# Optimization experiments

Hardware: AMD Instinct MI355X
Metric: run time of the kernel (lower is better)

## Reference

```python
import jax, jax.numpy as jnp
import numpy as np

DEPTH = 16
PERCENT = 1.2
MAX_P = 5.0
# ps[t] = clip((t+1)*percent, 0, max_percent), as in the torch __init__
PS = np.clip((np.arange(DEPTH) + 1) * PERCENT, 0.0, MAX_P)


def setup_inputs() -> dict:
    key = jax.random.key(0)
    kx, kA = jax.random.split(key, 2)
    B, M, N = 16384, 256, 1024
    A = jax.random.normal(kA, (M, N), dtype=jnp.float32) / np.sqrt(M)
    # L = max eigenvalue of A^T A (as max_eig in the torch code), scaled by 1.001
    gram = np.asarray(A.T @ A)
    L = float(np.linalg.eigvalsh(gram)[-1]) * 1.001
    # init=True initialization: every bias layer weight is A.T / L, threshold = 1/L
    W = jnp.tile((A.T / L)[None, :, :], (DEPTH, 1, 1))  # [depth, N, M]
    threshold = jnp.ones((DEPTH,), dtype=jnp.float32) / L
    x = jax.random.normal(kx, (B, M), dtype=jnp.float32)
    return {"x": x, "A": A, "W": W, "threshold": threshold}


def _shrink(x, t):
    # soft threshold: sign(x) * max(|x| - t, 0)
    return jnp.sign(x) * jnp.maximum(jnp.abs(x) - t, 0.0)


def _shrinkss(x, t, p):
    # support-selection shrink: entries above both the learned threshold and the
    # per-row (100-p) percentile of |x| pass through untouched; the rest are
    # soft-thresholded. Mask and percentile are detached (no_grad in torch).
    n = x.shape[1]
    idx = int(np.ceil((100.0 - p) / 100.0 * n)) - 1  # static per iteration
    abs_x = jnp.abs(x)
    thresh = jax.lax.stop_gradient(jnp.sort(abs_x, axis=1)[:, idx])  # [B]
    mask = jax.lax.stop_gradient(
        ((abs_x >= t) & (abs_x >= thresh[:, None])).astype(x.dtype)
    )
    return mask * x + _shrink((1.0 - mask) * x, t)


def reference(x, A, W, threshold):
    # x: [B, M], A: [M, N], W: [depth, N, M], threshold: [depth]
    B = x.shape[0]
    N = A.shape[1]
    u = jnp.zeros((B, N), dtype=x.dtype)
    for i in range(DEPTH):
        r = x - u @ A.T                      # residual in measurement space [B, M]
        v = u + r @ W[i].T                   # gradient step via learned bias [B, N]
        u = _shrinkss(v, threshold[i], PS[i])
    return u
```

## Files before the change

kernel.cpp:

```cpp
#include <hip/hip_runtime.h>
#include <hip/hip_bf16.h>

#define B_ROWS 16384
#define M_DIM  256
#define N_DIM  1024
#define DEPTH  16

typedef __attribute__((ext_vector_type(8))) short short8;
typedef __attribute__((ext_vector_type(4))) float f32x4;
typedef __attribute__((ext_vector_type(2))) float f32x2;

#define ATP_OFF_B   0
#define WTP_OFF_B   1572864
#define RP_OFF_B    (1572864 + 25165824)
#define TAU_OFF_B   (RP_OFF_B + 25165824)
#define WS_FAST_NEED ((size_t)TAU_OFF_B + 65536)
#define WTP_SLICE   (64 * 8 * 3 * 512)
#define RP_PANEL_US 24576

#define AT_OFF 0
#define WT_OFF (262144)
#define WS_OLD_NEED ((size_t)(262144 + 16 * 262144) * 4)

__device__ __forceinline__ unsigned short bf16r(float f) {
    unsigned u = __float_as_uint(f);
    u += 0x7fffu + ((u >> 16) & 1u);
    return (unsigned short)(u >> 16);
}
__device__ __forceinline__ float bf2f(unsigned short h) {
    return __uint_as_float(((unsigned)h) << 16);
}
__device__ __forceinline__ void split3(float x, unsigned short& h, unsigned short& m,
                                       unsigned short& lo) {
    h = bf16r(x); float r1 = x - bf2f(h);
    m = bf16r(r1); float r2 = r1 - bf2f(m);
    lo = bf16r(r2);
}
__device__ __forceinline__ f32x4 MF(short8 a, short8 b, f32x4 c) {
    return __builtin_amdgcn_mfma_f32_16x16x32_bf16(a, b, c, 0, 0, 0);
}
__device__ __forceinline__ float shrink_one(float v, float t, float thrv) {
    float a = fabsf(v);
    return (a >= thrv) ? v : copysignf(fmaxf(a - t, 0.0f), v);
}

__global__ void prep_a_kernel(const float* __restrict__ A, unsigned short* __restrict__ ATp) {
    int g = blockIdx.x * 256 + threadIdx.x;
    if (g >= 16 * 32 * 64) return;
    int l = g & 63, kc = (g >> 6) & 31, tile = g >> 11;
    int row = tile * 16 + (l & 15);
    int k0 = kc * 32 + ((l >> 4) << 3);
    unsigned short h[8], m[8], lo[8];
#pragma unroll
    for (int j = 0; j < 8; ++j) split3(A[(size_t)row * N_DIM + k0 + j], h[j], m[j], lo[j]);
    size_t base = ((size_t)(tile * 32 + kc) * 3) * 512 + l * 8;
#pragma unroll
    for (int j = 0; j < 8; ++j) {
        ATp[base + j] = h[j];
        ATp[base + 512 + j] = m[j];
        ATp[base + 1024 + j] = lo[j];
    }
}

__global__ void prep_w_kernel(const float* __restrict__ W, unsigned short* __restrict__ WTp) {
    int g = blockIdx.x * 256 + threadIdx.x;
    if (g >= 16 * 64 * 8 * 64) return;
    int l = g & 63, kc = (g >> 6) & 7, tile = (g >> 9) & 63, it = g >> 15;
    int n = tile * 16 + (l & 15);
    int m0 = kc * 32 + ((l >> 4) << 3);
    const float* Wi = W + (size_t)it * N_DIM * M_DIM;
    unsigned short h[8], m[8], lo[8];
#pragma unroll
    for (int j = 0; j < 8; ++j) split3(Wi[(size_t)n * M_DIM + m0 + j], h[j], m[j], lo[j]);
    size_t base = (((size_t)(it * 64 + tile) * 8 + kc) * 3) * 512 + l * 8;
#pragma unroll
    for (int j = 0; j < 8; ++j) {
        WTp[base + j] = h[j];
        WTp[base + 512 + j] = m[j];
        WTp[base + 1024 + j] = lo[j];
    }
}

__global__ void prep_x_kernel(const float* __restrict__ x, unsigned short* __restrict__ RP) {
    int g = blockIdx.x * 256 + threadIdx.x;
    if (g >= 524288) return;
    int l = g & 63, kcp = (g >> 6) & 3, wm = (g >> 8) & 1, c = (g >> 9) & 1, panel = g >> 10;
    int row = panel * 32 + wm * 16 + (l & 15);
    int k0 = c * 128 + kcp * 32 + ((l >> 4) << 3);
    unsigned short h[8], m[8], lo[8];
#pragma unroll
    for (int j = 0; j < 8; ++j) split3(x[(size_t)row * M_DIM + k0 + j], h[j], m[j], lo[j]);
    size_t base = (size_t)panel * RP_PANEL_US + ((((c * 2 + wm) * 4 + kcp) * 3)) * 512 + l * 8;
#pragma unroll
    for (int j = 0; j < 8; ++j) {
        RP[base + j] = h[j];
        RP[base + 512 + j] = m[j];
        RP[base + 1024 + j] = lo[j];
    }
}

#define LSTR2 136

__global__ __launch_bounds__(1024)
void g1_kernel(const float* __restrict__ UV, const float* __restrict__ x,
               const unsigned short* __restrict__ ATp,
               const float* __restrict__ thr_all, const float* __restrict__ TAU,
               unsigned short* __restrict__ RP, int iter) {
    __align__(16) __shared__ unsigned short smem[24576];
    const int tid = threadIdx.x;
    const int l = tid & 63, w = tid >> 6;
    const int wm = w >> 3, wn = w & 7;
    const int panel = blockIdx.x;
    const int row0 = panel * 32;
    const int arow = 16 * wm + (l & 15);
    const int akl  = (l >> 4) << 3;
    const float tprev = thr_all[iter - 1];

    f32x4 acc_hi[2], acc_rest[2];
    double acc64[2][4];
#pragma unroll
    for (int t = 0; t < 2; ++t) {
        acc_hi[t] = (f32x4){0, 0, 0, 0};
        acc_rest[t] = (f32x4){0, 0, 0, 0};
#pragma unroll
        for (int e = 0; e < 4; ++e) acc64[t][e] = 0.0;
    }

    f32x2 st[2];
#pragma unroll
    for (int jj = 0; jj < 2; ++jj) {
        const int idx = tid + 1024 * jj;
        const int r = idx >> 6, kq = idx & 63;
        st[jj] = *(const f32x2*)&UV[(size_t)(row0 + r) * N_DIM + kq * 2];
    }

    for (int c = 0; c < 8; ++c) {
        __syncthreads();
#pragma unroll
        for (int jj = 0; jj < 2; ++jj) {
            const int idx = tid + 1024 * jj;
            const int r = idx >> 6, kq = idx & 63;
            const float thrv = fmaxf(tprev, TAU[row0 + r]);
            const float a0 = shrink_one(st[jj].x, tprev, thrv);
            const float a1 = shrink_one(st[jj].y, tprev, thrv);
            unsigned short h0, m0, lo0, h1, m1, lo1;
            split3(a0, h0, m0, lo0);
            split3(a1, h1, m1, lo1);
            const unsigned off = (unsigned)r * LSTR2 + kq * 2;
            *(unsigned*)&smem[off] = (unsigned)h0 | ((unsigned)h1 << 16);
            *(unsigned*)&smem[4352 + off] = (unsigned)m0 | ((unsigned)m1 << 16);
            *(unsigned*)&smem[8704 + off] = (unsigned)lo0 | ((unsigned)lo1 << 16);
        }
        __syncthreads();
        if (c < 7) {
#pragma unroll
            for (int jj = 0; jj < 2; ++jj) {
                const int idx = tid + 1024 * jj;
                const int r = idx >> 6, kq = idx & 63;
                st[jj] = *(const f32x2*)&UV[(size_t)(row0 + r) * N_DIM + (c + 1) * 128 + kq * 2];
            }
        }
#pragma unroll
        for (int kc = 0; kc < 4; ++kc) {
            const unsigned ao = (unsigned)arow * LSTR2 + kc * 32 + akl;
            short8 ah = *(const short8*)&smem[ao];
            short8 am = *(const short8*)&smem[4352 + ao];
            short8 al = *(const short8*)&smem[8704 + ao];
#pragma unroll
            for (int tt = 0; tt < 2; ++tt) {
                const int tile = wn * 2 + tt;
                const unsigned bo = ((unsigned)(tile * 32 + c * 4 + kc) * 3) * 512 + l * 8;
                short8 bh = *(const short8*)&ATp[bo];
                short8 bm = *(const short8*)&ATp[bo + 512];
                short8 bl = *(const short8*)&ATp[bo + 1024];
                acc_hi[tt] = MF(ah, bh, acc_hi[tt]);
                acc_rest[tt] = MF(ah, bm, acc_rest[tt]);
                acc_rest[tt] = MF(am, bh, acc_rest[tt]);
                acc_rest[tt] = MF(am, bm, acc_rest[tt]);
                acc_rest[tt] = MF(ah, bl, acc_rest[tt]);
                acc_rest[tt] = MF(al, bh, acc_rest[tt]);
            }
        }
#pragma unroll
        for (int tt = 0; tt < 2; ++tt) {
#pragma unroll
            for (int e = 0; e < 4; ++e) acc64[tt][e] += (double)acc_hi[tt][e];
            acc_hi[tt] = (f32x4){0, 0, 0, 0};
        }
    }

    __syncthreads();
    {
        const int cimg = wn >> 2, kcp = wn & 3;
        const unsigned fbase = ((((unsigned)(cimg * 2 + wm) * 4 + kcp) * 3)) * 512;
#pragma unroll
        for (int tt = 0; tt < 2; ++tt) {
            const int col = wn * 32 + tt * 16 + (l & 15);
            const int hi2 = (tt * 2 + ((l & 15) >> 3)) & 3;
#pragma unroll
            for (int e = 0; e < 4; ++e) {
                const int rl = ((l >> 4) << 2) + e;
                const int row = row0 + wm * 16 + rl;
                const double tot = acc64[tt][e] + (double)acc_rest[tt][e];
                const float rv = (float)((double)x[(size_t)row * M_DIM + col] - tot);
                unsigned short h, m, lo;
                split3(rv, h, m, lo);
                const unsigned sl = fbase + (unsigned)(hi2 * 16 + rl) * 8 + (l & 7);
                smem[sl] = h;
                smem[sl + 512] = m;
                smem[sl + 1024] = lo;
            }
        }
    }
    __syncthreads();
    {
        const uint4* s4 = (const uint4*)smem;
        uint4* d4 = (uint4*)(RP + (size_t)panel * RP_PANEL_US);
        d4[tid] = s4[tid];
        d4[tid + 1024] = s4[tid + 1024];
        d4[tid + 2048] = s4[tid + 2048];
    }
}

__global__ __launch_bounds__(1024)
void g2_kernel(const unsigned short* __restrict__ RP, const unsigned short* __restrict__ WTpi,
               const float* __restrict__ thr_all, const float* __restrict__ TAU,
               float* UV, int iter) {
    __align__(16) __shared__ unsigned short img[24576];
    const int tid = threadIdx.x;
    const int l = tid & 63, w = tid >> 6;
    const int wm = w >> 3, wn = w & 7;
    const int panel = blockIdx.x >> 2, cg = blockIdx.x & 3;
    const int row0 = panel * 32;

    {
        const uint4* s4 = (const uint4*)(RP + (size_t)panel * RP_PANEL_US);
        uint4* d4 = (uint4*)img;
        d4[tid] = s4[tid];
        d4[tid + 1024] = s4[tid + 1024];
        d4[tid + 2048] = s4[tid + 2048];
    }
    __syncthreads();

    f32x4 hi[2], rest[2], sum[2];
#pragma unroll
    for (int t = 0; t < 2; ++t) {
        hi[t] = (f32x4){0, 0, 0, 0};
        rest[t] = (f32x4){0, 0, 0, 0};
        sum[t] = (f32x4){0, 0, 0, 0};
    }

    for (int kc = 0; kc < 8; ++kc) {
        const unsigned ab = ((((unsigned)(kc >> 2) * 2 + wm) * 4 + (kc & 3)) * 3) * 512 + l * 8;
        short8 ah = *(const short8*)&img[ab];
        short8 am = *(const short8*)&img[ab + 512];
        short8 al = *(const short8*)&img[ab + 1024];
#pragma unroll
        for (int tt = 0; tt < 2; ++tt) {
            const int tile = cg * 16 + wn * 2 + tt;
            const unsigned bo = ((unsigned)(tile * 8 + kc) * 3) * 512 + l * 8;
            short8 bh = *(const short8*)&WTpi[bo];
            short8 bm = *(const short8*)&WTpi[bo + 512];
            short8 bl = *(const short8*)&WTpi[bo + 1024];
            hi[tt] = MF(ah, bh, hi[tt]);
            rest[tt] = MF(ah, bm, rest[tt]);
            rest[tt] = MF(am, bh, rest[tt]);
            rest[tt] = MF(am, bm, rest[tt]);
            rest[tt] = MF(ah, bl, rest[tt]);
            rest[tt] = MF(al, bh, rest[tt]);
        }
        if ((kc & 3) == 3) {
#pragma unroll
            for (int tt = 0; tt < 2; ++tt) {
#pragma unroll
                for (int e = 0; e < 4; ++e) sum[tt][e] += hi[tt][e];
                hi[tt] = (f32x4){0, 0, 0, 0};
            }
        }
    }

    const float tprev = (iter > 0) ? thr_all[iter - 1] : 0.0f;
#pragma unroll
    for (int tt = 0; tt < 2; ++tt) {
        const int col = cg * 256 + wn * 32 + tt * 16 + (l & 15);
#pragma unroll
        for (int e = 0; e < 4; ++e) {
            const int row = row0 + wm * 16 + ((l >> 4) << 2) + e;
            const float tot = sum[tt][e] + rest[tt][e];
            float us = 0.0f;
            if (iter > 0) {
                const float uo = UV[(size_t)row * N_DIM + col];
                const float thrv = fmaxf(tprev, TAU[row]);
                us = shrink_one(uo, tprev, thrv);
            }
            UV[(size_t)row * N_DIM + col] = us + tot;
        }
    }
}

__global__ __launch_bounds__(1024)
void stau_kernel(const float* __restrict__ UV, float* __restrict__ TAU, int kth) {
    const int lane = threadIdx.x & 63;
    const int wave = threadIdx.x >> 6;
    const int row = blockIdx.x * 16 + wave;
    const float* vp = UV + (size_t)row * N_DIM;
    unsigned key[16];
#pragma unroll
    for (int j = 0; j < 16; ++j)
        key[j] = __float_as_uint(vp[lane + 64 * j]) & 0x7fffffffu;
    unsigned p = 0;
#pragma unroll 1
    for (int b = 30; b >= 0; --b) {
        const unsigned cand = p | (1u << b);
        int cnt = 0;
#pragma unroll
        for (int j = 0; j < 16; ++j) cnt += (key[j] >= cand) ? 1 : 0;
#pragma unroll
        for (int off = 32; off; off >>= 1) cnt += __shfl_xor(cnt, off);
        if (cnt >= kth) p = cand;
    }
    if (lane == 0) TAU[row] = __uint_as_float(p);
}

__global__ __launch_bounds__(256)
void s_kernel(float* UV, const float* __restrict__ thr_all, int iter, int kth) {
    __shared__ float v_s[8][1024];
    __shared__ float tau_s[8];
    const int tid = threadIdx.x;
    const int lane = tid & 63;
    const int wave = tid >> 6;
    const int row0 = blockIdx.x * 8;
    const float t = thr_all[iter];
    {
        const float4* Vg4 = (const float4*)(UV + (size_t)row0 * N_DIM);
        float4* vs4 = (float4*)(&v_s[0][0]);
#pragma unroll
        for (int c = 0; c < 8; ++c) vs4[tid + 256 * c] = Vg4[tid + 256 * c];
    }
    __syncthreads();
#pragma unroll 1
    for (int rr = 0; rr < 2; ++rr) {
        const int row = wave + rr * 4;
        unsigned key[16];
#pragma unroll
        for (int j = 0; j < 16; ++j)
            key[j] = __float_as_uint(v_s[row][lane + 64 * j]) & 0x7fffffffu;
        unsigned p = 0;
#pragma unroll 1
        for (int b = 30; b >= 0; --b) {
            const unsigned cand = p | (1u << b);
            int cnt = 0;
#pragma unroll
            for (int j = 0; j < 16; ++j) cnt += (key[j] >= cand) ? 1 : 0;
#pragma unroll
            for (int off = 32; off; off >>= 1) cnt += __shfl_xor(cnt, off);
            if (cnt >= kth) p = cand;
        }
        if (lane == 0) tau_s[row] = __uint_as_float(p);
    }
    __syncthreads();
    {
        const float4* vs4 = (const float4*)&v_s[0][0];
        float4* Uw = (float4*)(UV + (size_t)row0 * N_DIM);
#pragma unroll 1
        for (int c = 0; c < 8; ++c) {
            const int idx = tid + 256 * c;
            const int row = idx >> 8;
            const float thrv = fmaxf(t, tau_s[row]);
            float4 v = vs4[idx];
            float4 o;
            o.x = shrink_one(v.x, t, thrv);
            o.y = shrink_one(v.y, t, thrv);
            o.z = shrink_one(v.z, t, thrv);
            o.w = shrink_one(v.w, t, thrv);
            Uw[idx] = o;
        }
    }
}

#define DFMA4(acc, s, v) do { \
    (acc).x += (double)(s) * (double)(v).x; \
    (acc).y += (double)(s) * (double)(v).y; \
    (acc).z += (double)(s) * (double)(v).z; \
    (acc).w += (double)(s) * (double)(v).w; } while (0)

__global__ void transpose_kernel(const float* __restrict__ in, float* __restrict__ out,
                                 int R, int C) {
    __shared__ float tile[32][33];
    int s = blockIdx.z;
    const float* ip = in + (size_t)s * R * C;
    float* op = out + (size_t)s * R * C;
    int c0 = blockIdx.x * 32, r0 = blockIdx.y * 32;
    int tx = threadIdx.x, ty = threadIdx.y;
#pragma unroll
    for (int k = 0; k < 4; ++k)
        tile[ty + 8 * k][tx] = ip[(size_t)(r0 + ty + 8 * k) * C + (c0 + tx)];
    __syncthreads();
#pragma unroll
    for (int k = 0; k < 4; ++k)
        op[(size_t)(c0 + ty + 8 * k) * R + (r0 + tx)] = tile[tx][ty + 8 * k];
}

__global__ void zero_kernel(float* __restrict__ p, int n) {
    int i = blockIdx.x * blockDim.x + threadIdx.x;
    int stride = gridDim.x * blockDim.x;
    for (; i < n; i += stride) p[i] = 0.0f;
}

template <bool T>
__device__ __forceinline__ float4 loadAT(const float* __restrict__ p, int n, int m4) {
    if constexpr (T) {
        return ((const float4*)p)[n * 64 + m4];
    } else {
        float4 r;
        r.x = p[(size_t)(4 * m4 + 0) * N_DIM + n];
        r.y = p[(size_t)(4 * m4 + 1) * N_DIM + n];
        r.z = p[(size_t)(4 * m4 + 2) * N_DIM + n];
        r.w = p[(size_t)(4 * m4 + 3) * N_DIM + n];
        return r;
    }
}
template <bool T>
__device__ __forceinline__ float4 loadWT(const float* __restrict__ p, int m, int n4) {
    if constexpr (T) {
        return ((const float4*)p)[m * 256 + n4];
    } else {
        float4 r;
        r.x = p[(size_t)(4 * n4 + 0) * M_DIM + m];
        r.y = p[(size_t)(4 * n4 + 1) * M_DIM + m];
        r.z = p[(size_t)(4 * n4 + 2) * M_DIM + m];
        r.w = p[(size_t)(4 * n4 + 3) * M_DIM + m];
        return r;
    }
}

template <bool T>
__global__ __launch_bounds__(256)
void lista_iter_kernel(const float* __restrict__ x, const float* __restrict__ Ap,
                       const float* __restrict__ Wp, const float* __restrict__ thr_all,
                       float* __restrict__ U, int iter, int kth) {
    __shared__ float u_s[8][1024];
    __shared__ float r_s[8][256];
    __shared__ float tau_s[8];
    const int tid = threadIdx.x;
    const int lane = tid & 63;
    const int wave = tid >> 6;
    const int row0 = blockIdx.x * 8;
    const float t = thr_all[iter];
    {
        const float4* Ug4 = (const float4*)(U + (size_t)row0 * N_DIM);
        float4* us4 = (float4*)(&u_s[0][0]);
#pragma unroll
        for (int c = 0; c < 8; ++c) us4[tid + 256 * c] = Ug4[tid + 256 * c];
    }
    __syncthreads();
    {
        double4 acc0 = {0, 0, 0, 0}, acc1 = {0, 0, 0, 0};
        const float4* u0p = (const float4*)&u_s[wave][0];
        const float4* u1p = (const float4*)&u_s[wave + 4][0];
        for (int n4 = 0; n4 < 256; ++n4) {
            float4 u0 = u0p[n4];
            float4 u1 = u1p[n4];
            float4 a0 = loadAT<T>(Ap, 4 * n4 + 0, lane);
            float4 a1 = loadAT<T>(Ap, 4 * n4 + 1, lane);
            float4 a2 = loadAT<T>(Ap, 4 * n4 + 2, lane);
            float4 a3 = loadAT<T>(Ap, 4 * n4 + 3, lane);
            DFMA4(acc0, u0.x, a0); DFMA4(acc0, u0.y, a1); DFMA4(acc0, u0.z, a2); DFMA4(acc0, u0.w, a3);
            DFMA4(acc1, u1.x, a0); DFMA4(acc1, u1.y, a1); DFMA4(acc1, u1.z, a2); DFMA4(acc1, u1.w, a3);
        }
        float4 xv0 = ((const float4*)(x + (size_t)(row0 + wave) * M_DIM))[lane];
        float4 xv1 = ((const float4*)(x + (size_t)(row0 + wave + 4) * M_DIM))[lane];
        float4 rv0, rv1;
        rv0.x = (float)((double)xv0.x - acc0.x);
        rv0.y = (float)((double)xv0.y - acc0.y);
        rv0.z = (float)((double)xv0.z - acc0.z);
        rv0.w = (float)((double)xv0.w - acc0.w);
        rv1.x = (float)((double)xv1.x - acc1.x);
        rv1.y = (float)((double)xv1.y - acc1.y);
        rv1.z = (float)((double)xv1.z - acc1.z);
        rv1.w = (float)((double)xv1.w - acc1.w);
        ((float4*)&r_s[wave][0])[lane] = rv0;
        ((float4*)&r_s[wave + 4][0])[lane] = rv1;
    }
    __syncthreads();
    {
        const float4* r0p = (const float4*)&r_s[wave][0];
        const float4* r1p = (const float4*)&r_s[wave + 4][0];
        float4* u0p = (float4*)&u_s[wave][0];
        float4* u1p = (float4*)&u_s[wave + 4][0];
#pragma unroll 1
        for (int q = 0; q < 4; ++q) {
            const int n4 = lane + 64 * q;
            double4 acc0 = {0, 0, 0, 0}, acc1 = {0, 0, 0, 0};
            for (int m4 = 0; m4 < 64; ++m4) {
                float4 r0 = r0p[m4];
                float4 r1 = r1p[m4];
                float4 w0 = loadWT<T>(Wp, 4 * m4 + 0, n4);
                float4 w1 = loadWT<T>(Wp, 4 * m4 + 1, n4);
                float4 w2 = loadWT<T>(Wp, 4 * m4 + 2, n4);
                float4 w3 = loadWT<T>(Wp, 4 * m4 + 3, n4);
                DFMA4(acc0, r0.x, w0); DFMA4(acc0, r0.y, w1); DFMA4(acc0, r0.z, w2); DFMA4(acc0, r0.w, w3);
                DFMA4(acc1, r1.x, w0); DFMA4(acc1, r1.y, w1); DFMA4(acc1, r1.z, w2); DFMA4(acc1, r1.w, w3);
            }
            float4 uv0 = u0p[n4];
            uv0.x = (float)((double)uv0.x + acc0.x);
            uv0.y = (float)((double)uv0.y + acc0.y);
            uv0.z = (float)((double)uv0.z + acc0.z);
            uv0.w = (float)((double)uv0.w + acc0.w);
            u0p[n4] = uv0;
            float4 uv1 = u1p[n4];
            uv1.x = (float)((double)uv1.x + acc1.x);
            uv1.y = (float)((double)uv1.y + acc1.y);
            uv1.z = (float)((double)uv1.z + acc1.z);
            uv1.w = (float)((double)uv1.w + acc1.w);
            u1p[n4] = uv1;
        }
    }
    __syncthreads();
    {
#pragma unroll 1
        for (int rr = 0; rr < 2; ++rr) {
            const int row = wave + rr * 4;
            unsigned key[16];
#pragma unroll
            for (int j = 0; j < 16; ++j)
                key[j] = __float_as_uint(u_s[row][lane + 64 * j]) & 0x7fffffffu;
            unsigned p = 0;
#pragma unroll 1
            for (int b = 30; b >= 0; --b) {
                const unsigned cand = p | (1u << b);
                int cnt = 0;
#pragma unroll
                for (int j = 0; j < 16; ++j) cnt += (key[j] >= cand) ? 1 : 0;
#pragma unroll
                for (int off = 32; off; off >>= 1) cnt += __shfl_xor(cnt, off);
                if (cnt >= kth) p = cand;
            }
            if (lane == 0) tau_s[row] = __uint_as_float(p);
        }
    }
    __syncthreads();
    {
        const float4* us4 = (const float4*)&u_s[0][0];
        float4* Uw = (float4*)(U + (size_t)row0 * N_DIM);
#pragma unroll 1
        for (int c = 0; c < 8; ++c) {
            const int idx = tid + 256 * c;
            const int row = idx >> 8;
            const float thrv = fmaxf(t, tau_s[row]);
            float4 v = us4[idx];
            float4 o;
            o.x = shrink_one(v.x, t, thrv);
            o.y = shrink_one(v.y, t, thrv);
            o.z = shrink_one(v.z, t, thrv);
            o.w = shrink_one(v.w, t, thrv);
            Uw[idx] = o;
        }
    }
}

extern "C" void kernel_launch(void* const* d_in, const int* in_sizes, int n_in,
                              void* d_out, int out_size, void* d_ws, size_t ws_size,
                              hipStream_t stream) {
    const float* x   = (const float*)d_in[0];
    const float* A   = (const float*)d_in[1];
    const float* W   = (const float*)d_in[2];
    const float* thr = (const float*)d_in[3];

    float* UV = (float*)d_out;

    static const int ktab[DEPTH] = {13, 25, 37, 50, 52, 52, 52, 52,
                                    52, 52, 52, 52, 52, 52, 52, 52};

    if (ws_size >= WS_FAST_NEED) {
        unsigned short* ATp = (unsigned short*)((char*)d_ws + ATP_OFF_B);
        unsigned short* WTp = (unsigned short*)((char*)d_ws + WTP_OFF_B);
        unsigned short* RP  = (unsigned short*)((char*)d_ws + RP_OFF_B);
        float* TAU = (float*)((char*)d_ws + TAU_OFF_B);

        prep_a_kernel<<<128, 256, 0, stream>>>(A, ATp);
        prep_w_kernel<<<2048, 256, 0, stream>>>(W, WTp);
        prep_x_kernel<<<2048, 256, 0, stream>>>(x, RP);

        g2_kernel<<<2048, 1024, 0, stream>>>(RP, WTp, thr, TAU, UV, 0);
        stau_kernel<<<B_ROWS / 16, 1024, 0, stream>>>(UV, TAU, ktab[0]);

        for (int it = 1; it < DEPTH; ++it) {
            g1_kernel<<<512, 1024, 0, stream>>>(UV, x, ATp, thr, TAU, RP, it);
            g2_kernel<<<2048, 1024, 0, stream>>>(RP, WTp + (size_t)it * WTP_SLICE,
                                                 thr, TAU, UV, it);
            if (it < DEPTH - 1)
                stau_kernel<<<B_ROWS / 16, 1024, 0, stream>>>(UV, TAU, ktab[it]);
            else
                s_kernel<<<B_ROWS / 8, 256, 0, stream>>>(UV, thr, it, ktab[it]);
        }
    } else if (ws_size >= WS_OLD_NEED) {
        float* ws = (float*)d_ws;
        float* AT = ws + AT_OFF;
        float* WT = ws + WT_OFF;
        zero_kernel<<<1024, 256, 0, stream>>>(UV, B_ROWS * N_DIM);
        dim3 tb(32, 8);
        transpose_kernel<<<dim3(N_DIM / 32, M_DIM / 32, 1), tb, 0, stream>>>(A, AT, M_DIM, N_DIM);
        transpose_kernel<<<dim3(M_DIM / 32, N_DIM / 32, DEPTH), tb, 0, stream>>>(W, WT, N_DIM, M_DIM);
        for (int it = 0; it < DEPTH; ++it)
            lista_iter_kernel<true><<<B_ROWS / 8, 256, 0, stream>>>(
                x, AT, WT + (size_t)it * M_DIM * N_DIM, thr, UV, it, ktab[it]);
    } else {
        zero_kernel<<<1024, 256, 0, stream>>>(UV, B_ROWS * N_DIM);
        for (int it = 0; it < DEPTH; ++it)
            lista_iter_kernel<false><<<B_ROWS / 8, 256, 0, stream>>>(
                x, A, W + (size_t)it * N_DIM * M_DIM, thr, UV, it, ktab[it]);
    }
}
```

Baseline: 3.172 ms.

## Fuse all LISTA iterations into one persistent per-row-block mega kernel

Replaces the per-iteration g1/g2/stau/s kernel sequence with a single kernel in which each 512-thread block owns 16 rows. The block keeps the iterate u in registers across all 16 depths, computes the residual and gradient GEMMs from shared memory, and does the per-row percentile selection with ballot/popcount. This removes the global round trips for UV, RP and TAU plus about 50 kernel launches. In exchange it runs only 1024 smaller blocks with heavy register pressure and many __syncthreads, and every block re-reads the A and W panels from L2.

```diff
diff --git a/kernel.cpp b/kernel.cpp
--- a/kernel.cpp
+++ b/kernel.cpp
@@ -8,15 +8,11 @@
 
 typedef __attribute__((ext_vector_type(8))) short short8;
 typedef __attribute__((ext_vector_type(4))) float f32x4;
-typedef __attribute__((ext_vector_type(2))) float f32x2;
 
 #define ATP_OFF_B   0
 #define WTP_OFF_B   1572864
-#define RP_OFF_B    (1572864 + 25165824)
-#define TAU_OFF_B   (RP_OFF_B + 25165824)
-#define WS_FAST_NEED ((size_t)TAU_OFF_B + 65536)
+#define WS_FAST_NEED ((size_t)WTP_OFF_B + 25165824)
 #define WTP_SLICE   (64 * 8 * 3 * 512)
-#define RP_PANEL_US 24576
 
 #define AT_OFF 0
 #define WT_OFF (262144)
@@ -81,300 +77,226 @@
     }
 }
 
-__global__ void prep_x_kernel(const float* __restrict__ x, unsigned short* __restrict__ RP) {
-    int g = blockIdx.x * 256 + threadIdx.x;
-    if (g >= 524288) return;
-    int l = g & 63, kcp = (g >> 6) & 3, wm = (g >> 8) & 1, c = (g >> 9) & 1, panel = g >> 10;
-    int row = panel * 32 + wm * 16 + (l & 15);
-    int k0 = c * 128 + kcp * 32 + ((l >> 4) << 3);
-    unsigned short h[8], m[8], lo[8];
-#pragma unroll
-    for (int j = 0; j < 8; ++j) split3(x[(size_t)row * M_DIM + k0 + j], h[j], m[j], lo[j]);
-    size_t base = (size_t)panel * RP_PANEL_US + ((((c * 2 + wm) * 4 + kcp) * 3)) * 512 + l * 8;
-#pragma unroll
-    for (int j = 0; j < 8; ++j) {
-        RP[base + j] = h[j];
-        RP[base + 512 + j] = m[j];
-        RP[base + 1024 + j] = lo[j];
-    }
-}
-
-#define LSTR2 136
-
-__global__ __launch_bounds__(1024)
-void g1_kernel(const float* __restrict__ UV, const float* __restrict__ x,
-               const unsigned short* __restrict__ ATp,
-               const float* __restrict__ thr_all, const float* __restrict__ TAU,
-               unsigned short* __restrict__ RP, int iter) {
-    __align__(16) __shared__ unsigned short smem[24576];
+__global__ __launch_bounds__(512)
+void mega_kernel(const float* __restrict__ x, const unsigned short* __restrict__ ATp,
+                 const unsigned short* __restrict__ WTp, const float* __restrict__ thr_all,
+                 float* __restrict__ UV) {
+    __align__(16) __shared__ unsigned short smem[30336];
+    float* vbuf = (float*)&smem[26112];
     const int tid = threadIdx.x;
     const int l = tid & 63, w = tid >> 6;
-    const int wm = w >> 3, wn = w & 7;
-    const int panel = blockIdx.x;
-    const int row0 = panel * 32;
-    const int arow = 16 * wm + (l & 15);
+    const int row0 = blockIdx.x * 16;
+    const int arow = l & 15;
     const int akl  = (l >> 4) << 3;
-    const float tprev = thr_all[iter - 1];
-
-    f32x4 acc_hi[2], acc_rest[2];
-    double acc64[2][4];
-#pragma unroll
-    for (int t = 0; t < 2; ++t) {
-        acc_hi[t] = (f32x4){0, 0, 0, 0};
-        acc_rest[t] = (f32x4){0, 0, 0, 0};
-#pragma unroll
-        for (int e = 0; e < 4; ++e) acc64[t][e] = 0.0;
-    }
-
-    f32x2 st[2];
-#pragma unroll
-    for (int jj = 0; jj < 2; ++jj) {
-        const int idx = tid + 1024 * jj;
-        const int r = idx >> 6, kq = idx & 63;
-        st[jj] = *(const f32x2*)&UV[(size_t)(row0 + r) * N_DIM + kq * 2];
-    }
-
-    for (int c = 0; c < 8; ++c) {
-        __syncthreads();
-#pragma unroll
-        for (int jj = 0; jj < 2; ++jj) {
-            const int idx = tid + 1024 * jj;
-            const int r = idx >> 6, kq = idx & 63;
-            const float thrv = fmaxf(tprev, TAU[row0 + r]);
-            const float a0 = shrink_one(st[jj].x, tprev, thrv);
-            const float a1 = shrink_one(st[jj].y, tprev, thrv);
-            unsigned short h0, m0, lo0, h1, m1, lo1;
-            split3(a0, h0, m0, lo0);
-            split3(a1, h1, m1, lo1);
-            const unsigned off = (unsigned)r * LSTR2 + kq * 2;
-            *(unsigned*)&smem[off] = (unsigned)h0 | ((unsigned)h1 << 16);
-            *(unsigned*)&smem[4352 + off] = (unsigned)m0 | ((unsigned)m1 << 16);
-            *(unsigned*)&smem[8704 + off] = (unsigned)lo0 | ((unsigned)lo1 << 16);
-        }
-        __syncthreads();
-        if (c < 7) {
+
+    float u0[16], u1[16];
+#pragma unroll
+    for (int j = 0; j < 16; ++j) { u0[j] = 0.0f; u1[j] = 0.0f; }
+
+#pragma unroll 1
+    for (int it = 0; it < DEPTH; ++it) {
+        if (it == 0) {
+            const int kcp = (tid >> 6) & 3, cc = (tid >> 8) & 1;
+            const int row = row0 + (l & 15);
+            const int k0 = cc * 128 + kcp * 32 + akl;
+            const unsigned base = ((unsigned)(cc * 4 + kcp) * 3) * 512 + (unsigned)l * 8;
+#pragma unroll
+            for (int j = 0; j < 8; ++j) {
+                unsigned short h, m, lo;
+                split3(x[(size_t)row * M_DIM + k0 + j], h, m, lo);
+                smem[base + j] = h;
+                smem[base + 512 + j] = m;
+                smem[base + 1024 + j] = lo;
+            }
+            __syncthreads();
+        } else {
+            f32x4 acc_hi[2], acc_rest[2];
+            double acc64[2][4];
+#pragma unroll
+            for (int t = 0; t < 2; ++t) {
+                acc_hi[t] = (f32x4){0, 0, 0, 0};
+                acc_rest[t] = (f32x4){0, 0, 0, 0};
+#pragma unroll
+                for (int e = 0; e < 4; ++e) acc64[t][e] = 0.0;
+            }
+            float xr[2][4];
+#pragma unroll
+            for (int tt = 0; tt < 2; ++tt) {
+                const int col = (w * 2 + tt) * 16 + (l & 15);
+#pragma unroll
+                for (int e = 0; e < 4; ++e) {
+                    const int mi = ((l >> 4) << 2) + e;
+                    xr[tt][e] = x[(size_t)(row0 + mi) * M_DIM + col];
+                }
+            }
+#pragma unroll
+            for (int rr = 0; rr < 2; ++rr) {
+#pragma unroll
+                for (int jj = 0; jj < 2; ++jj) {
+                    const float uval = rr ? u1[jj] : u0[jj];
+                    unsigned short h, m, lo;
+                    split3(uval, h, m, lo);
+                    const unsigned off = (unsigned)(2 * w + rr) * 136 + l + 64 * jj;
+                    smem[off] = h;
+                    smem[off + 2176] = m;
+                    smem[off + 4352] = lo;
+                }
+            }
+            __syncthreads();
+#pragma unroll
+            for (int c = 0; c < 8; ++c) {
+                const unsigned bb = (c & 1) ? 6528u : 0u;
+                if (c < 7) {
+                    const unsigned nb = (c & 1) ? 0u : 6528u;
+#pragma unroll
+                    for (int rr = 0; rr < 2; ++rr) {
+#pragma unroll
+                        for (int jj = 0; jj < 2; ++jj) {
+                            const float uval = rr ? u1[2 * (c + 1) + jj] : u0[2 * (c + 1) + jj];
+                            unsigned short h, m, lo;
+                            split3(uval, h, m, lo);
+                            const unsigned off = nb + (unsigned)(2 * w + rr) * 136 + l + 64 * jj;
+                            smem[off] = h;
+                            smem[off + 2176] = m;
+                            smem[off + 4352] = lo;
+                        }
+                    }
+                }
+#pragma unroll
+                for (int kc = 0; kc < 4; ++kc) {
+                    const unsigned ao = bb + (unsigned)arow * 136 + kc * 32 + akl;
+                    short8 ah = *(const short8*)&smem[ao];
+                    short8 am = *(const short8*)&smem[ao + 2176];
+                    short8 al = *(const short8*)&smem[ao + 4352];
+#pragma unroll
+                    for (int tt = 0; tt < 2; ++tt) {
+                        const int tile = w * 2 + tt;
+                        const unsigned bo = ((unsigned)(tile * 32 + c * 4 + kc) * 3) * 512 + l * 8;
+                        short8 bh = *(const short8*)&ATp[bo];
+                        short8 bm = *(const short8*)&ATp[bo + 512];
+                        short8 bl = *(const short8*)&ATp[bo + 1024];
+                        acc_hi[tt] = MF(ah, bh, acc_hi[tt]);
+                        acc_rest[tt] = MF(ah, bm, acc_rest[tt]);
+                        acc_rest[tt] = MF(am, bh, acc_rest[tt]);
+                        acc_rest[tt] = MF(am, bm, acc_rest[tt]);
+                        acc_rest[tt] = MF(ah, bl, acc_rest[tt]);
+                        acc_rest[tt] = MF(al, bh, acc_rest[tt]);
+                    }
+                }
+#pragma unroll
+                for (int tt = 0; tt < 2; ++tt) {
+#pragma unroll
+                    for (int e = 0; e < 4; ++e) acc64[tt][e] += (double)acc_hi[tt][e];
+                    acc_hi[tt] = (f32x4){0, 0, 0, 0};
+                }
+                __syncthreads();
+            }
+#pragma unroll
+            for (int tt = 0; tt < 2; ++tt) {
+                const int ki = (w * 2 + tt) * 16 + (l & 15);
+                const unsigned slb = ((unsigned)(ki >> 5) * 3) * 512 +
+                                     ((unsigned)((ki >> 3) & 3) * 16) * 8 + (ki & 7);
+#pragma unroll
+                for (int e = 0; e < 4; ++e) {
+                    const int mi = ((l >> 4) << 2) + e;
+                    const double tot = acc64[tt][e] + (double)acc_rest[tt][e];
+                    const float rv = (float)((double)xr[tt][e] - tot);
+                    unsigned short h, m, lo;
+                    split3(rv, h, m, lo);
+                    const unsigned sl = slb + (unsigned)mi * 8;
+                    smem[sl] = h;
+                    smem[sl + 512] = m;
+                    smem[sl + 1024] = lo;
+                }
+            }
+            __syncthreads();
+        }
+
+        const unsigned short* WTpi = WTp + (size_t)it * WTP_SLICE;
+#pragma unroll
+        for (int g = 0; g < 8; ++g) {
+            f32x4 hi = (f32x4){0, 0, 0, 0};
+            f32x4 rest = (f32x4){0, 0, 0, 0};
+            f32x4 sum = (f32x4){0, 0, 0, 0};
+            const int tile = g * 8 + w;
+#pragma unroll
+            for (int kc = 0; kc < 8; ++kc) {
+                const unsigned ab = ((unsigned)kc * 3) * 512 + l * 8;
+                short8 ah = *(const short8*)&smem[ab];
+                short8 am = *(const short8*)&smem[ab + 512];
+                short8 al = *(const short8*)&smem[ab + 1024];
+                const unsigned bo = ((unsigned)(tile * 8 + kc) * 3) * 512 + l * 8;
+                short8 bh = *(const short8*)&WTpi[bo];
+                short8 bm = *(const short8*)&WTpi[bo + 512];
+                short8 bl = *(const short8*)&WTpi[bo + 1024];
+                hi = MF(ah, bh, hi);
+                rest = MF(ah, bm, rest);
+                rest = MF(am, bh, rest);
+                rest = MF(am, bm, rest);
+                rest = MF(ah, bl, rest);
+                rest = MF(al, bh, rest);
+                if ((kc & 3) == 3) {
+#pragma unroll
+                    for (int e = 0; e < 4; ++e) sum[e] += hi[e];
+                    hi = (f32x4){0, 0, 0, 0};
+                }
+            }
+#pragma unroll
+            for (int e = 0; e < 4; ++e) {
+                const int mi = ((l >> 4) << 2) + e;
+                vbuf[mi * 132 + w * 16 + (l & 15)] = sum[e] + rest[e];
+            }
+            __syncthreads();
 #pragma unroll
             for (int jj = 0; jj < 2; ++jj) {
-                const int idx = tid + 1024 * jj;
-                const int r = idx >> 6, kq = idx & 63;
-                st[jj] = *(const f32x2*)&UV[(size_t)(row0 + r) * N_DIM + (c + 1) * 128 + kq * 2];
-            }
-        }
-#pragma unroll
-        for (int kc = 0; kc < 4; ++kc) {
-            const unsigned ao = (unsigned)arow * LSTR2 + kc * 32 + akl;
-            short8 ah = *(const short8*)&smem[ao];
-            short8 am = *(const short8*)&smem[4352 + ao];
-            short8 al = *(const short8*)&smem[8704 + ao];
-#pragma unroll
-            for (int tt = 0; tt < 2; ++tt) {
-                const int tile = wn * 2 + tt;
-                const unsigned bo = ((unsigned)(tile * 32 + c * 4 + kc) * 3) * 512 + l * 8;
-                short8 bh = *(const short8*)&ATp[bo];
-                short8 bm = *(const short8*)&ATp[bo + 512];
-                short8 bl = *(const short8*)&ATp[bo + 1024];
-                acc_hi[tt] = MF(ah, bh, acc_hi[tt]);
-                acc_rest[tt] = MF(ah, bm, acc_rest[tt]);
-                acc_rest[tt] = MF(am, bh, acc_rest[tt]);
-                acc_rest[tt] = MF(am, bm, acc_rest[tt]);
-                acc_rest[tt] = MF(ah, bl, acc_rest[tt]);
-                acc_rest[tt] = MF(al, bh, acc_rest[tt]);
-            }
-        }
-#pragma unroll
-        for (int tt = 0; tt < 2; ++tt) {
-#pragma unroll
-            for (int e = 0; e < 4; ++e) acc64[tt][e] += (double)acc_hi[tt][e];
-            acc_hi[tt] = (f32x4){0, 0, 0, 0};
-        }
-    }
-
-    __syncthreads();
-    {
-        const int cimg = wn >> 2, kcp = wn & 3;
-        const unsigned fbase = ((((unsigned)(cimg * 2 + wm) * 4 + kcp) * 3)) * 512;
-#pragma unroll
-        for (int tt = 0; tt < 2; ++tt) {
-            const int col = wn * 32 + tt * 16 + (l & 15);
-            const int hi2 = (tt * 2 + ((l & 15) >> 3)) & 3;
-#pragma unroll
-            for (int e = 0; e < 4; ++e) {
-                const int rl = ((l >> 4) << 2) + e;
-                const int row = row0 + wm * 16 + rl;
-                const double tot = acc64[tt][e] + (double)acc_rest[tt][e];
-                const float rv = (float)((double)x[(size_t)row * M_DIM + col] - tot);
-                unsigned short h, m, lo;
-                split3(rv, h, m, lo);
-                const unsigned sl = fbase + (unsigned)(hi2 * 16 + rl) * 8 + (l & 7);
-                smem[sl] = h;
-                smem[sl + 512] = m;
-                smem[sl + 1024] = lo;
-            }
-        }
-    }
-    __syncthreads();
-    {
-        const uint4* s4 = (const uint4*)smem;
-        uint4* d4 = (uint4*)(RP + (size_t)panel * RP_PANEL_US);
-        d4[tid] = s4[tid];
-        d4[tid + 1024] = s4[tid + 1024];
-        d4[tid + 2048] = s4[tid + 2048];
-    }
-}
-
-__global__ __launch_bounds__(1024)
-void g2_kernel(const unsigned short* __restrict__ RP, const unsigned short* __restrict__ WTpi,
-               const float* __restrict__ thr_all, const float* __restrict__ TAU,
-               float* UV, int iter) {
-    __align__(16) __shared__ unsigned short img[24576];
-    const int tid = threadIdx.x;
-    const int l = tid & 63, w = tid >> 6;
-    const int wm = w >> 3, wn = w & 7;
-    const int panel = blockIdx.x >> 2, cg = blockIdx.x & 3;
-    const int row0 = panel * 32;
-
-    {
-        const uint4* s4 = (const uint4*)(RP + (size_t)panel * RP_PANEL_US);
-        uint4* d4 = (uint4*)img;
-        d4[tid] = s4[tid];
-        d4[tid + 1024] = s4[tid + 1024];
-        d4[tid + 2048] = s4[tid + 2048];
-    }
-    __syncthreads();
-
-    f32x4 hi[2], rest[2], sum[2];
-#pragma unroll
-    for (int t = 0; t < 2; ++t) {
-        hi[t] = (f32x4){0, 0, 0, 0};
-        rest[t] = (f32x4){0, 0, 0, 0};
-        sum[t] = (f32x4){0, 0, 0, 0};
-    }
-
-    for (int kc = 0; kc < 8; ++kc) {
-        const unsigned ab = ((((unsigned)(kc >> 2) * 2 + wm) * 4 + (kc & 3)) * 3) * 512 + l * 8;
-        short8 ah = *(const short8*)&img[ab];
-        short8 am = *(const short8*)&img[ab + 512];
-        short8 al = *(const short8*)&img[ab + 1024];
-#pragma unroll
-        for (int tt = 0; tt < 2; ++tt) {
-            const int tile = cg * 16 + wn * 2 + tt;
-            const unsigned bo = ((unsigned)(tile * 8 + kc) * 3) * 512 + l * 8;
-            short8 bh = *(const short8*)&WTpi[bo];
-            short8 bm = *(const short8*)&WTpi[bo + 512];
-            short8 bl = *(const short8*)&WTpi[bo + 1024];
-            hi[tt] = MF(ah, bh, hi[tt]);
-            rest[tt] = MF(ah, bm, rest[tt]);
-            rest[tt] = MF(am, bh, rest[tt]);
-            rest[tt] = MF(am, bm, rest[tt]);
-            rest[tt] = MF(ah, bl, rest[tt]);
-            rest[tt] = MF(al, bh, rest[tt]);
-        }
-        if ((kc & 3) == 3) {
-#pragma unroll
-            for (int tt = 0; tt < 2; ++tt) {
-#pragma unroll
-                for (int e = 0; e < 4; ++e) sum[tt][e] += hi[tt][e];
-                hi[tt] = (f32x4){0, 0, 0, 0};
-            }
-        }
-    }
-
-    const float tprev = (iter > 0) ? thr_all[iter - 1] : 0.0f;
-#pragma unroll
-    for (int tt = 0; tt < 2; ++tt) {
-        const int col = cg * 256 + wn * 32 + tt * 16 + (l & 15);
-#pragma unroll
-        for (int e = 0; e < 4; ++e) {
-            const int row = row0 + wm * 16 + ((l >> 4) << 2) + e;
-            const float tot = sum[tt][e] + rest[tt][e];
-            float us = 0.0f;
-            if (iter > 0) {
-                const float uo = UV[(size_t)row * N_DIM + col];
-                const float thrv = fmaxf(tprev, TAU[row]);
-                us = shrink_one(uo, tprev, thrv);
-            }
-            UV[(size_t)row * N_DIM + col] = us + tot;
-        }
-    }
-}
-
-__global__ __launch_bounds__(1024)
-void stau_kernel(const float* __restrict__ UV, float* __restrict__ TAU, int kth) {
-    const int lane = threadIdx.x & 63;
-    const int wave = threadIdx.x >> 6;
-    const int row = blockIdx.x * 16 + wave;
-    const float* vp = UV + (size_t)row * N_DIM;
-    unsigned key[16];
-#pragma unroll
-    for (int j = 0; j < 16; ++j)
-        key[j] = __float_as_uint(vp[lane + 64 * j]) & 0x7fffffffu;
-    unsigned p = 0;
-#pragma unroll 1
-    for (int b = 30; b >= 0; --b) {
-        const unsigned cand = p | (1u << b);
-        int cnt = 0;
-#pragma unroll
-        for (int j = 0; j < 16; ++j) cnt += (key[j] >= cand) ? 1 : 0;
-#pragma unroll
-        for (int off = 32; off; off >>= 1) cnt += __shfl_xor(cnt, off);
-        if (cnt >= kth) p = cand;
-    }
-    if (lane == 0) TAU[row] = __uint_as_float(p);
-}
-
-__global__ __launch_bounds__(256)
-void s_kernel(float* UV, const float* __restrict__ thr_all, int iter, int kth) {
-    __shared__ float v_s[8][1024];
-    __shared__ float tau_s[8];
-    const int tid = threadIdx.x;
-    const int lane = tid & 63;
-    const int wave = tid >> 6;
-    const int row0 = blockIdx.x * 8;
-    const float t = thr_all[iter];
-    {
-        const float4* Vg4 = (const float4*)(UV + (size_t)row0 * N_DIM);
-        float4* vs4 = (float4*)(&v_s[0][0]);
-#pragma unroll
-        for (int c = 0; c < 8; ++c) vs4[tid + 256 * c] = Vg4[tid + 256 * c];
-    }
-    __syncthreads();
-#pragma unroll 1
-    for (int rr = 0; rr < 2; ++rr) {
-        const int row = wave + rr * 4;
-        unsigned key[16];
-#pragma unroll
-        for (int j = 0; j < 16; ++j)
-            key[j] = __float_as_uint(v_s[row][lane + 64 * j]) & 0x7fffffffu;
-        unsigned p = 0;
-#pragma unroll 1
-        for (int b = 30; b >= 0; --b) {
-            const unsigned cand = p | (1u << b);
-            int cnt = 0;
-#pragma unroll
-            for (int j = 0; j < 16; ++j) cnt += (key[j] >= cand) ? 1 : 0;
-#pragma unroll
-            for (int off = 32; off; off >>= 1) cnt += __shfl_xor(cnt, off);
-            if (cnt >= kth) p = cand;
-        }
-        if (lane == 0) tau_s[row] = __uint_as_float(p);
-    }
-    __syncthreads();
-    {
-        const float4* vs4 = (const float4*)&v_s[0][0];
-        float4* Uw = (float4*)(UV + (size_t)row0 * N_DIM);
-#pragma unroll 1
-        for (int c = 0; c < 8; ++c) {
-            const int idx = tid + 256 * c;
-            const int row = idx >> 8;
-            const float thrv = fmaxf(t, tau_s[row]);
-            float4 v = vs4[idx];
-            float4 o;
-            o.x = shrink_one(v.x, t, thrv);
-            o.y = shrink_one(v.y, t, thrv);
-            o.z = shrink_one(v.z, t, thrv);
-            o.w = shrink_one(v.w, t, thrv);
-            Uw[idx] = o;
-        }
+                u0[g * 2 + jj] += vbuf[(2 * w) * 132 + l + 64 * jj];
+                u1[g * 2 + jj] += vbuf[(2 * w + 1) * 132 + l + 64 * jj];
+            }
+            __syncthreads();
+        }
+
+        const float t = thr_all[it];
+        const int kth = (it >= 4) ? 52 : ((it == 3) ? 50 : 13 + 12 * it);
+        {
+            unsigned key[16];
+#pragma unroll
+            for (int j = 0; j < 16; ++j) key[j] = __float_as_uint(u0[j]) & 0x7fffffffu;
+            unsigned p = 0;
+#pragma unroll 1
+            for (int b = 30; b >= 0; --b) {
+                const unsigned cand = p | (1u << b);
+                int cnt = 0;
+#pragma unroll
+                for (int j = 0; j < 16; ++j) cnt += __popcll(__ballot(key[j] >= cand));
+                if (cnt >= kth) p = cand;
+            }
+            const float thrv = fmaxf(t, __uint_as_float(p));
+#pragma unroll
+            for (int j = 0; j < 16; ++j) u0[j] = shrink_one(u0[j], t, thrv);
+        }
+        {
+            unsigned key[16];
+#pragma unroll
+            for (int j = 0; j < 16; ++j) key[j] = __float_as_uint(u1[j]) & 0x7fffffffu;
+            unsigned p = 0;
+#pragma unroll 1
+            for (int b = 30; b >= 0; --b) {
+                const unsigned cand = p | (1u << b);
+                int cnt = 0;
+#pragma unroll
+                for (int j = 0; j < 16; ++j) cnt += __popcll(__ballot(key[j] >= cand));
+                if (cnt >= kth) p = cand;
+            }
+            const float thrv = fmaxf(t, __uint_as_float(p));
+#pragma unroll
+            for (int j = 0; j < 16; ++j) u1[j] = shrink_one(u1[j], t, thrv);
+        }
+    }
+
+#pragma unroll
+    for (int j = 0; j < 16; ++j) {
+        UV[(size_t)(row0 + 2 * w) * N_DIM + l + 64 * j] = u0[j];
+        UV[(size_t)(row0 + 2 * w + 1) * N_DIM + l + 64 * j] = u1[j];
     }
 }
 
@@ -575,25 +497,10 @@
     if (ws_size >= WS_FAST_NEED) {
         unsigned short* ATp = (unsigned short*)((char*)d_ws + ATP_OFF_B);
         unsigned short* WTp = (unsigned short*)((char*)d_ws + WTP_OFF_B);
-        unsigned short* RP  = (unsigned short*)((char*)d_ws + RP_OFF_B);
-        float* TAU = (float*)((char*)d_ws + TAU_OFF_B);
 
         prep_a_kernel<<<128, 256, 0, stream>>>(A, ATp);
         prep_w_kernel<<<2048, 256, 0, stream>>>(W, WTp);
-        prep_x_kernel<<<2048, 256, 0, stream>>>(x, RP);
-
-        g2_kernel<<<2048, 1024, 0, stream>>>(RP, WTp, thr, TAU, UV, 0);
-        stau_kernel<<<B_ROWS / 16, 1024, 0, stream>>>(UV, TAU, ktab[0]);
-
-        for (int it = 1; it < DEPTH; ++it) {
-            g1_kernel<<<512, 1024, 0, stream>>>(UV, x, ATp, thr, TAU, RP, it);
-            g2_kernel<<<2048, 1024, 0, stream>>>(RP, WTp + (size_t)it * WTP_SLICE,
-                                                 thr, TAU, UV, it);
-            if (it < DEPTH - 1)
-                stau_kernel<<<B_ROWS / 16, 1024, 0, stream>>>(UV, TAU, ktab[it]);
-            else
-                s_kernel<<<B_ROWS / 8, 256, 0, stream>>>(UV, thr, it, ktab[it]);
-        }
+        mega_kernel<<<B_ROWS / 16, 512, 0, stream>>>(x, ATp, WTp, thr, UV);
     } else if (ws_size >= WS_OLD_NEED) {
         float* ws = (float*)d_ws;
         float* AT = ws + AT_OFF;
```

Result: slower. 4.041 ms (+27.4%).

## Double-buffer g1 LDS staging and use ballot-popcount in stau radix select

Applied to the files above, without the earlier changes.

g1_kernel now keeps two LDS buffers for the shrunk, three-way-split UV chunk. The next chunk is converted into the spare buffer while MFMAs run on the current one, so each chunk step has one barrier instead of two. Per-thread offsets and thresholds are hoisted out of the loop. stau_kernel counts with wave ballot plus popcount instead of per-lane counts and a shuffle reduction, and the launch loop is reordered without changing semantics. The cost is double the LDS footprint for g1 and more live registers.

```diff
diff --git a/kernel.cpp b/kernel.cpp
--- a/kernel.cpp
+++ b/kernel.cpp
@@ -99,14 +99,38 @@
     }
 }
 
+__global__ __launch_bounds__(1024)
+void stau_kernel(const float* __restrict__ UV, float* __restrict__ TAU, int kth) {
+    const int l = threadIdx.x & 63;
+    const int w = threadIdx.x >> 6;
+    const int row = blockIdx.x * 16 + w;
+    const float* vp = UV + (size_t)row * N_DIM;
+    unsigned key[16];
+#pragma unroll
+    for (int j = 0; j < 16; ++j)
+        key[j] = __float_as_uint(vp[l + 64 * j]) & 0x7fffffffu;
+    unsigned p = 0;
+#pragma unroll 1
+    for (int b = 30; b >= 0; --b) {
+        const unsigned cand = p | (1u << b);
+        int cnt = 0;
+#pragma unroll
+        for (int j = 0; j < 16; ++j)
+            cnt += __popcll(__ballot(key[j] >= cand));
+        if (cnt >= kth) p = cand;
+    }
+    if (l == 0) TAU[row] = __uint_as_float(p);
+}
+
 #define LSTR2 136
+#define BUFUS 13056
 
 __global__ __launch_bounds__(1024)
 void g1_kernel(const float* __restrict__ UV, const float* __restrict__ x,
                const unsigned short* __restrict__ ATp,
                const float* __restrict__ thr_all, const float* __restrict__ TAU,
                unsigned short* __restrict__ RP, int iter) {
-    __align__(16) __shared__ unsigned short smem[24576];
+    __align__(16) __shared__ unsigned short smem[2 * BUFUS];
     const int tid = threadIdx.x;
     const int l = tid & 63, w = tid >> 6;
     const int wm = w >> 3, wn = w & 7;
@@ -126,46 +150,60 @@
         for (int e = 0; e < 4; ++e) acc64[t][e] = 0.0;
     }
 
-    f32x2 st[2];
+    unsigned soff[2]; float thrv_r[2]; const float* uvp[2];
 #pragma unroll
     for (int jj = 0; jj < 2; ++jj) {
         const int idx = tid + 1024 * jj;
         const int r = idx >> 6, kq = idx & 63;
-        st[jj] = *(const f32x2*)&UV[(size_t)(row0 + r) * N_DIM + kq * 2];
-    }
+        soff[jj] = (unsigned)r * LSTR2 + kq * 2;
+        thrv_r[jj] = fmaxf(tprev, TAU[row0 + r]);
+        uvp[jj] = UV + (size_t)(row0 + r) * N_DIM + kq * 2;
+    }
+
+    f32x2 st[2];
+#pragma unroll
+    for (int jj = 0; jj < 2; ++jj) st[jj] = *(const f32x2*)(uvp[jj]);
+#pragma unroll
+    for (int jj = 0; jj < 2; ++jj) {
+        const float a0 = shrink_one(st[jj].x, tprev, thrv_r[jj]);
+        const float a1 = shrink_one(st[jj].y, tprev, thrv_r[jj]);
+        unsigned short h0, m0, lo0, h1, m1, lo1;
+        split3(a0, h0, m0, lo0);
+        split3(a1, h1, m1, lo1);
+        *(unsigned*)&smem[soff[jj]] = (unsigned)h0 | ((unsigned)h1 << 16);
+        *(unsigned*)&smem[4352 + soff[jj]] = (unsigned)m0 | ((unsigned)m1 << 16);
+        *(unsigned*)&smem[8704 + soff[jj]] = (unsigned)lo0 | ((unsigned)lo1 << 16);
+    }
+#pragma unroll
+    for (int jj = 0; jj < 2; ++jj) st[jj] = *(const f32x2*)(uvp[jj] + 128);
+    __syncthreads();
 
     for (int c = 0; c < 8; ++c) {
-        __syncthreads();
-#pragma unroll
-        for (int jj = 0; jj < 2; ++jj) {
-            const int idx = tid + 1024 * jj;
-            const int r = idx >> 6, kq = idx & 63;
-            const float thrv = fmaxf(tprev, TAU[row0 + r]);
-            const float a0 = shrink_one(st[jj].x, tprev, thrv);
-            const float a1 = shrink_one(st[jj].y, tprev, thrv);
-            unsigned short h0, m0, lo0, h1, m1, lo1;
-            split3(a0, h0, m0, lo0);
-            split3(a1, h1, m1, lo1);
-            const unsigned off = (unsigned)r * LSTR2 + kq * 2;
-            *(unsigned*)&smem[off] = (unsigned)h0 | ((unsigned)h1 << 16);
-            *(unsigned*)&smem[4352 + off] = (unsigned)m0 | ((unsigned)m1 << 16);
-            *(unsigned*)&smem[8704 + off] = (unsigned)lo0 | ((unsigned)lo1 << 16);
-        }
-        __syncthreads();
+        const unsigned bb = (unsigned)(c & 1) * BUFUS;
+        const unsigned nb = (unsigned)((c + 1) & 1) * BUFUS;
         if (c < 7) {
 #pragma unroll
             for (int jj = 0; jj < 2; ++jj) {
-                const int idx = tid + 1024 * jj;
-                const int r = idx >> 6, kq = idx & 63;
-                st[jj] = *(const f32x2*)&UV[(size_t)(row0 + r) * N_DIM + (c + 1) * 128 + kq * 2];
+                const float a0 = shrink_one(st[jj].x, tprev, thrv_r[jj]);
+                const float a1 = shrink_one(st[jj].y, tprev, thrv_r[jj]);
+                unsigned short h0, m0, lo0, h1, m1, lo1;
+                split3(a0, h0, m0, lo0);
+                split3(a1, h1, m1, lo1);
+                *(unsigned*)&smem[nb + soff[jj]] = (unsigned)h0 | ((unsigned)h1 << 16);
+                *(unsigned*)&smem[nb + 4352 + soff[jj]] = (unsigned)m0 | ((unsigned)m1 << 16);
+                *(unsigned*)&smem[nb + 8704 + soff[jj]] = (unsigned)lo0 | ((unsigned)lo1 << 16);
             }
         }
+        if (c < 6) {
+#pragma unroll
+            for (int jj = 0; jj < 2; ++jj) st[jj] = *(const f32x2*)(uvp[jj] + (c + 2) * 128);
+        }
 #pragma unroll
         for (int kc = 0; kc < 4; ++kc) {
-            const unsigned ao = (unsigned)arow * LSTR2 + kc * 32 + akl;
+            const unsigned ao = bb + (unsigned)arow * LSTR2 + kc * 32 + akl;
             short8 ah = *(const short8*)&smem[ao];
-            short8 am = *(const short8*)&smem[4352 + ao];
-            short8 al = *(const short8*)&smem[8704 + ao];
+            short8 am = *(const short8*)&smem[ao + 4352];
+            short8 al = *(const short8*)&smem[ao + 8704];
 #pragma unroll
             for (int tt = 0; tt < 2; ++tt) {
                 const int tile = wn * 2 + tt;
@@ -187,9 +225,9 @@
             for (int e = 0; e < 4; ++e) acc64[tt][e] += (double)acc_hi[tt][e];
             acc_hi[tt] = (f32x4){0, 0, 0, 0};
         }
-    }
-
-    __syncthreads();
+        __syncthreads();
+    }
+
     {
         const int cimg = wn >> 2, kcp = wn & 3;
         const unsigned fbase = ((((unsigned)(cimg * 2 + wm) * 4 + kcp) * 3)) * 512;
@@ -296,30 +334,6 @@
             UV[(size_t)row * N_DIM + col] = us + tot;
         }
     }
-}
-
-__global__ __launch_bounds__(1024)
-void stau_kernel(const float* __restrict__ UV, float* __restrict__ TAU, int kth) {
-    const int lane = threadIdx.x & 63;
-    const int wave = threadIdx.x >> 6;
-    const int row = blockIdx.x * 16 + wave;
-    const float* vp = UV + (size_t)row * N_DIM;
-    unsigned key[16];
-#pragma unroll
-    for (int j = 0; j < 16; ++j)
-        key[j] = __float_as_uint(vp[lane + 64 * j]) & 0x7fffffffu;
-    unsigned p = 0;
-#pragma unroll 1
-    for (int b = 30; b >= 0; --b) {
-        const unsigned cand = p | (1u << b);
-        int cnt = 0;
-#pragma unroll
-        for (int j = 0; j < 16; ++j) cnt += (key[j] >= cand) ? 1 : 0;
-#pragma unroll
-        for (int off = 32; off; off >>= 1) cnt += __shfl_xor(cnt, off);
-        if (cnt >= kth) p = cand;
-    }
-    if (lane == 0) TAU[row] = __uint_as_float(p);
 }
 
 __global__ __launch_bounds__(256)
@@ -583,17 +597,14 @@
         prep_x_kernel<<<2048, 256, 0, stream>>>(x, RP);
 
         g2_kernel<<<2048, 1024, 0, stream>>>(RP, WTp, thr, TAU, UV, 0);
-        stau_kernel<<<B_ROWS / 16, 1024, 0, stream>>>(UV, TAU, ktab[0]);
 
         for (int it = 1; it < DEPTH; ++it) {
+            stau_kernel<<<B_ROWS / 16, 1024, 0, stream>>>(UV, TAU, ktab[it - 1]);
             g1_kernel<<<512, 1024, 0, stream>>>(UV, x, ATp, thr, TAU, RP, it);
             g2_kernel<<<2048, 1024, 0, stream>>>(RP, WTp + (size_t)it * WTP_SLICE,
                                                  thr, TAU, UV, it);
-            if (it < DEPTH - 1)
-                stau_kernel<<<B_ROWS / 16, 1024, 0, stream>>>(UV, TAU, ktab[it]);
-            else
-                s_kernel<<<B_ROWS / 8, 256, 0, stream>>>(UV, thr, it, ktab[it]);
-        }
+        }
+        s_kernel<<<B_ROWS / 8, 256, 0, stream>>>(UV, thr, DEPTH - 1, ktab[DEPTH - 1]);
     } else if (ws_size >= WS_OLD_NEED) {
         float* ws = (float*)d_ws;
         float* AT = ws + AT_OFF;
```

After: 2.955 ms (median of 2 runs). -6.9%, faster.
